# Optimization experiments

Hardware: AMD Instinct MI355X
Metric: run time of the kernel (lower is better)

Reference implementation:

```python
import jax, jax.numpy as jnp
import numpy as np

B, TED, G, N, E, MD, NOISE = 10000, 512, 64, 2000, 64000, 15, 128
PAC = 10
PACDIM = (TED + NOISE) * PAC  # 6400
D0, D1 = 1024, 512


def _linear_params(k, fan_in, fan_out):
    kw, kb = jax.random.split(k)
    lim = 1.0 / np.sqrt(fan_in)
    w = jax.random.uniform(kw, (fan_in, fan_out), minval=-lim, maxval=lim, dtype=jnp.float32)
    b = jax.random.uniform(kb, (fan_out,), minval=-lim, maxval=lim, dtype=jnp.float32)
    return w, b


def setup_inputs() -> dict:
    key = jax.random.key(0)
    ks = jax.random.split(key, 12)
    inp = {
        'input_': jax.random.normal(ks[0], (B, TED), dtype=jnp.float32),
        'graphs_x': jax.random.normal(ks[1], (G, N, 1), dtype=jnp.float32),
        'edge_index': jax.random.randint(ks[2], (G, 2, E), 0, N, dtype=jnp.int32),
        'graph_ids': jax.random.randint(ks[3], (B,), 0, G, dtype=jnp.int32),
        'chain': jax.random.normal(ks[4], (B, 1), dtype=jnp.float32),
        'metadata': jax.random.normal(ks[5], (B, MD), dtype=jnp.float32),
    }
    inp['gcn_w'], inp['gcn_b'] = _linear_params(ks[6], 1, 1)
    inp['meta_w'], inp['meta_b'] = _linear_params(ks[7], 1 + MD, 32)
    inp['gme_w'], inp['gme_b'] = _linear_params(ks[8], N + 32, NOISE)
    inp['seq_w0'], inp['seq_b0'] = _linear_params(ks[9], PACDIM, D0)
    inp['seq_w1'], inp['seq_b1'] = _linear_params(ks[10], D0, D1)
    inp['seq_w2'], inp['seq_b2'] = _linear_params(ks[11], D1, 1)
    return inp


def _gcn_one(x, ei, gcn_w, gcn_b):
    # GCNConv(1,1) with self-loops and symmetric normalization.
    loops = jnp.arange(N, dtype=ei.dtype)
    src = jnp.concatenate([ei[0], loops])
    dst = jnp.concatenate([ei[1], loops])
    deg = jax.ops.segment_sum(jnp.ones_like(src, dtype=x.dtype), dst, num_segments=N)
    dinv = jax.lax.rsqrt(deg)  # deg >= 1 due to self-loops
    norm = dinv[src] * dinv[dst]  # [E+N]
    xw = x @ gcn_w  # [N,1]
    msg = xw[src] * norm[:, None]
    out = jax.ops.segment_sum(msg, dst, num_segments=N) + gcn_b
    return out.reshape(-1)  # flatten -> [N]


def reference(input_, graphs_x, edge_index, graph_ids, chain, metadata,
              gcn_w, gcn_b, meta_w, meta_b, gme_w, gme_b,
              seq_w0, seq_b0, seq_w1, seq_b1, seq_w2, seq_b2):
    # per-unique-graph GCN, vectorized over G graphs
    gcn_out = jax.vmap(lambda x, ei: _gcn_one(x, ei, gcn_w, gcn_b))(graphs_x, edge_index)  # [G,N]
    graph_emb = gcn_out[graph_ids]  # gather: [B,N]
    all_meta = jnp.concatenate([chain, metadata], axis=1)  # [B,1+MD]
    meta_emb = jax.nn.relu(all_meta @ meta_w + meta_b)  # [B,32]
    noise = jnp.concatenate([graph_emb, meta_emb], axis=1) @ gme_w + gme_b  # [B,NOISE]
    h = jnp.concatenate([input_, noise], axis=1).reshape(-1, PACDIM)  # [B/PAC, PACDIM]
    h = jax.nn.leaky_relu(h @ seq_w0 + seq_b0, 0.2)  # dropout omitted (eval mode)
    h = jax.nn.leaky_relu(h @ seq_w1 + seq_b1, 0.2)
    return h @ seq_w2 + seq_b2  # [B/PAC, 1]
```

## Files before the change

kernel.cpp:

```cpp
#include <hip/hip_runtime.h>

typedef __bf16 bf16_t;
typedef __bf16 bf16x4 __attribute__((ext_vector_type(4)));
typedef __bf16 bf16x8 __attribute__((ext_vector_type(8)));
typedef float floatx4 __attribute__((ext_vector_type(4)));

#define G_GRAPHS 64
#define N_NODES 2000
#define N_EDGES 64000
#define BATCH 10000
#define TED_ 512
#define NOISE_ 128
#define PACDIM_ 6400
#define D0_ 1024
#define D1_ 512
#define MROWS 1000
#define ESPLIT 8
#define EPB (N_EDGES / ESPLIT)
#define S0 10
#define S1 8

#define PACK_BLKS 5000
#define META_BLKS 2500
#define TW0_BLKS  6400
#define TW1_BLKS  512

__device__ __forceinline__ void glds16(const void* g, void* l) {
    __builtin_amdgcn_global_load_lds(
        (__attribute__((address_space(1))) void*)(g),
        (__attribute__((address_space(3))) void*)(l), 16, 0, 0);
}

__global__ __launch_bounds__(256) void zero_kernel(float4* __restrict__ p, int n4) {
    int i = blockIdx.x * 256 + threadIdx.x;
    if (i < n4) p[i] = make_float4(0.f, 0.f, 0.f, 0.f);
}

__global__ __launch_bounds__(512) void deg_kernel(
    const int* __restrict__ edge_index, float* __restrict__ degs)
{
    __shared__ float h[N_NODES];
    const int g = blockIdx.y, s = blockIdx.x, tid = threadIdx.x;
    for (int n = tid; n < N_NODES; n += 512) h[n] = 0.f;
    __syncthreads();
    const int* dst = edge_index + (size_t)g * 2 * N_EDGES + N_EDGES + s * EPB;
    for (int e = tid; e < EPB; e += 512) atomicAdd(&h[dst[e]], 1.0f);
    __syncthreads();
    float* dg = degs + (size_t)g * N_NODES;
    for (int n = tid; n < N_NODES; n += 512) {
        float v = h[n];
        if (v != 0.f) atomicAdd(&dg[n], v);
    }
}

__global__ __launch_bounds__(512) void msg_kernel(
    const float* __restrict__ graphs_x, const int* __restrict__ edge_index,
    const float* __restrict__ degs, float* __restrict__ outs)
{
    __shared__ float xsl[N_NODES];
    __shared__ float dvl[N_NODES];
    __shared__ float oh[N_NODES];
    const int g = blockIdx.y, s = blockIdx.x, tid = threadIdx.x;
    const float* xg = graphs_x + (size_t)g * N_NODES;
    const float* dgg = degs + (size_t)g * N_NODES;
    for (int n = tid; n < N_NODES; n += 512) {
        xsl[n] = xg[n];
        dvl[n] = rsqrtf(dgg[n] + 1.0f);
        oh[n] = 0.f;
    }
    __syncthreads();
    const int* src = edge_index + (size_t)g * 2 * N_EDGES + s * EPB;
    const int* dst = src + N_EDGES;
    for (int e = tid; e < EPB; e += 512) {
        int ss = src[e], dd = dst[e];
        atomicAdd(&oh[dd], xsl[ss] * dvl[ss] * dvl[dd]);
    }
    __syncthreads();
    float* og = outs + (size_t)g * N_NODES;
    for (int n = tid; n < N_NODES; n += 512) {
        float v = oh[n];
        if (v != 0.f) atomicAdd(&og[n], v);
    }
}

__global__ __launch_bounds__(512) void gnoise_part_kernel(
    const float* __restrict__ graphs_x, const float* __restrict__ degs,
    const float* __restrict__ outs,
    const float* __restrict__ gcn_w, const float* __restrict__ gcn_b,
    const float* __restrict__ gme_w, float* __restrict__ gnoise)
{
    __shared__ float of[500];
    __shared__ float part[4][128];
    const int s = blockIdx.x, g = blockIdx.y, tid = threadIdx.x;
    const int nBase = s * 500;
    const float w = gcn_w[0], b = gcn_b[0];
    for (int n = tid; n < 500; n += 512) {
        int gn = nBase + n;
        float di2 = 1.0f / (degs[(size_t)g * N_NODES + gn] + 1.0f);
        of[n] = w * (outs[(size_t)g * N_NODES + gn]
                     + graphs_x[(size_t)g * N_NODES + gn] * di2) + b;
    }
    __syncthreads();
    const int j = tid & 127, ch = tid >> 7;
    float acc = 0.f;
    const int n0 = ch * 125;
    for (int n = n0; n < n0 + 125; n++)
        acc += of[n] * gme_w[(size_t)(nBase + n) * 128 + j];
    part[ch][j] = acc;
    __syncthreads();
    if (tid < 128)
        atomicAdd(&gnoise[(size_t)g * 128 + tid],
                  part[0][tid] + part[1][tid] + part[2][tid] + part[3][tid]);
}

__global__ __launch_bounds__(256) void prep_kernel(
    const float* __restrict__ in,
    const float* __restrict__ chain, const float* __restrict__ metadata,
    const int* __restrict__ graph_ids,
    const float* __restrict__ meta_w, const float* __restrict__ meta_b,
    const float* __restrict__ gme_w, const float* __restrict__ gme_b,
    const float* __restrict__ gnoise, bf16_t* __restrict__ A,
    const float* __restrict__ seq_w0, bf16_t* __restrict__ W0t,
    const float* __restrict__ seq_w1, bf16_t* __restrict__ W1t)
{
    __shared__ float t[32][33];
    const int blk = blockIdx.x;
    if (blk < PACK_BLKS) {
        int idx = blk * 256 + threadIdx.x;
        float4 v = ((const float4*)in)[idx];
        int b = idx >> 7;
        int c = (idx & 127) << 2;
        int r = b / 10, slot = b - r * 10;
        bf16x4 o = { (bf16_t)v.x, (bf16_t)v.y, (bf16_t)v.z, (bf16_t)v.w };
        *(bf16x4*)(A + (size_t)r * PACDIM_ + slot * 640 + c) = o;
        return;
    }
    if (blk < PACK_BLKS + META_BLKS) {
        int wid = ((blk - PACK_BLKS) * 256 + threadIdx.x) >> 6;
        int lane = threadIdx.x & 63;
        const int b = wid;
        float me = 0.f;
        if (lane < 32) {
            me = meta_b[lane] + chain[b] * meta_w[lane];
            for (int i = 1; i < 16; i++)
                me += metadata[(size_t)b * 15 + (i - 1)] * meta_w[(size_t)i * 32 + lane];
            me = me > 0.f ? me : 0.f;
        }
        const int gid = graph_ids[b];
        const int j1 = lane, j2 = lane + 64;
        float n1 = gnoise[(size_t)gid * 128 + j1] + gme_b[j1];
        float n2 = gnoise[(size_t)gid * 128 + j2] + gme_b[j2];
        for (int k = 0; k < 32; k++) {
            float mk = __shfl(me, k, 64);
            const float* wrow = gme_w + (size_t)(N_NODES + k) * 128;
            n1 += mk * wrow[j1];
            n2 += mk * wrow[j2];
        }
        int r = b / 10, slot = b - r * 10;
        bf16_t* dp = A + (size_t)r * PACDIM_ + slot * 640 + TED_;
        dp[j1] = (bf16_t)n1;
        dp[j2] = (bf16_t)n2;
        return;
    }
    const float* W; bf16_t* Wt; int R, C, c0, r0;
    if (blk < PACK_BLKS + META_BLKS + TW0_BLKS) {
        int local = blk - PACK_BLKS - META_BLKS;
        W = seq_w0; Wt = W0t; R = PACDIM_; C = D0_;
        c0 = (local & 31) * 32; r0 = (local >> 5) * 32;
    } else {
        int local = blk - PACK_BLKS - META_BLKS - TW0_BLKS;
        W = seq_w1; Wt = W1t; R = D0_; C = D1_;
        c0 = (local & 15) * 32; r0 = (local >> 4) * 32;
    }
    int tx = threadIdx.x & 31, ty = threadIdx.x >> 5;
    for (int yy = ty; yy < 32; yy += 8)
        t[yy][tx] = W[(size_t)(r0 + yy) * C + c0 + tx];
    __syncthreads();
    for (int yy = ty; yy < 32; yy += 8)
        Wt[(size_t)(c0 + yy) * R + r0 + tx] = (bf16_t)t[tx][yy];
}

__global__ __launch_bounds__(256) void gemm_bt_splitk_kernel(
    const bf16_t* __restrict__ A,
    const bf16_t* __restrict__ Bt,
    float* __restrict__ P,
    int M, int N, int K, int KS)
{
    __shared__ __align__(16) bf16_t As[128 * 32];
    __shared__ __align__(16) bf16_t Bs[128 * 32];
    const int tid = threadIdx.x;
    const int wave = tid >> 6;
    const int lane = tid & 63;
    const int mBase = blockIdx.y * 128;
    const int nBase = blockIdx.x * 128;
    const int z = blockIdx.z;
    const int Mp = gridDim.y * 128;
    const int wm = (wave & 1) * 64;
    const int wn = (wave >> 1) * 64;

    floatx4 acc[4][4] = {};

    const int c0 = tid, c1 = tid + 256;
    const int rA0 = c0 >> 2, k80 = (c0 & 3) * 8;
    const int rA1 = c1 >> 2, k81 = (c1 & 3) * 8;
    int gm0 = mBase + rA0; if (gm0 > M - 1) gm0 = M - 1;
    int gm1 = mBase + rA1; if (gm1 > M - 1) gm1 = M - 1;
    const bf16_t* aP0 = A + (size_t)gm0 * K + k80;
    const bf16_t* aP1 = A + (size_t)gm1 * K + k81;
    const bf16_t* bP0 = Bt + (size_t)(nBase + rA0) * K + k80;
    const bf16_t* bP1 = Bt + (size_t)(nBase + rA1) * K + k81;
    char* lA0 = (char*)As + wave * 1024;
    char* lA1 = (char*)As + 4096 + wave * 1024;
    char* lB0 = (char*)Bs + wave * 1024;
    char* lB1 = (char*)Bs + 4096 + wave * 1024;

    const int kq = (lane >> 4) * 8;
    const int mr = lane & 15;
    const bf16x8* ra[4]; const bf16x8* rb[4];
    for (int i = 0; i < 4; i++)
        ra[i] = (const bf16x8*)&As[(wm + i * 16 + mr) * 32 + kq];
    for (int j = 0; j < 4; j++)
        rb[j] = (const bf16x8*)&Bs[(wn + j * 16 + mr) * 32 + kq];

    const int kEnd = z * KS + KS;
    for (int k0 = z * KS; k0 < kEnd; k0 += 32) {
        __syncthreads();
        glds16(aP0 + k0, lA0);
        glds16(aP1 + k0, lA1);
        glds16(bP0 + k0, lB0);
        glds16(bP1 + k0, lB1);
        __syncthreads();
        bf16x8 af[4], bfr[4];
        for (int i = 0; i < 4; i++) af[i] = *ra[i];
        for (int j = 0; j < 4; j++) bfr[j] = *rb[j];
        for (int i = 0; i < 4; i++)
            for (int j = 0; j < 4; j++)
                acc[i][j] = __builtin_amdgcn_mfma_f32_16x16x32_bf16(
                    af[i], bfr[j], acc[i][j], 0, 0, 0);
    }

    float* Pz = P + (size_t)z * Mp * N;
    const int rq = (lane >> 4) * 4;
    const int cn = lane & 15;
    for (int j = 0; j < 4; j++) {
        int col = nBase + wn + j * 16 + cn;
        for (int i = 0; i < 4; i++)
            for (int r = 0; r < 4; r++) {
                int rowm = mBase + wm + i * 16 + rq + r;
                Pz[(size_t)rowm * N + col] = acc[i][j][r];
            }
    }
}

__global__ __launch_bounds__(256) void reduce_bias_leaky_kernel(
    const float* __restrict__ P, const float* __restrict__ bias,
    bf16_t* __restrict__ C, int M, int N, int Mp, int S)
{
    int idx = blockIdx.x * 256 + threadIdx.x;
    int total = M * (N >> 2);
    if (idx >= total) return;
    int nv = N >> 2;
    int r = idx / nv, c4 = (idx - r * nv) << 2;
    size_t off = (size_t)r * N + c4;
    size_t stride = (size_t)Mp * N;
    float4 v = *(const float4*)(P + off);
    for (int s = 1; s < S; s++) {
        float4 u = *(const float4*)(P + s * stride + off);
        v.x += u.x; v.y += u.y; v.z += u.z; v.w += u.w;
    }
    const float4 bv = *(const float4*)(bias + c4);
    v.x += bv.x; v.y += bv.y; v.z += bv.z; v.w += bv.w;
    v.x = v.x > 0.f ? v.x : 0.2f * v.x;
    v.y = v.y > 0.f ? v.y : 0.2f * v.y;
    v.z = v.z > 0.f ? v.z : 0.2f * v.z;
    v.w = v.w > 0.f ? v.w : 0.2f * v.w;
    bf16x4 o = { (bf16_t)v.x, (bf16_t)v.y, (bf16_t)v.z, (bf16_t)v.w };
    *(bf16x4*)(C + off) = o;
}

__global__ __launch_bounds__(256) void final_fused_kernel(
    const float* __restrict__ P, const float* __restrict__ b1,
    const float* __restrict__ w2, const float* __restrict__ b2,
    float* __restrict__ out, int Mp, int S)
{
    int wid = (blockIdx.x * 256 + threadIdx.x) >> 6;
    int lane = threadIdx.x & 63;
    if (wid >= MROWS) return;
    size_t stride = (size_t)Mp * D1_;
    const float* base = P + (size_t)wid * D1_;
    float s = 0.f;
    for (int i = 0; i < 8; i++) {
        int c = i * 64 + lane;
        float v = base[c];
        for (int z = 1; z < S; z++) v += base[(size_t)z * stride + c];
        v += b1[c];
        v = v > 0.f ? v : 0.2f * v;
        s += v * w2[c];
    }
    for (int off = 32; off; off >>= 1) s += __shfl_down(s, off, 64);
    if (lane == 0) out[wid] = s + b2[0];
}

extern "C" void kernel_launch(void* const* d_in, const int* in_sizes, int n_in,
                              void* d_out, int out_size, void* d_ws, size_t ws_size,
                              hipStream_t stream)
{
    const float* input_    = (const float*)d_in[0];
    const float* graphs_x  = (const float*)d_in[1];
    const int*   edge_idx  = (const int*)  d_in[2];
    const int*   graph_ids = (const int*)  d_in[3];
    const float* chain     = (const float*)d_in[4];
    const float* metadata  = (const float*)d_in[5];
    const float* gcn_w     = (const float*)d_in[6];
    const float* gcn_b     = (const float*)d_in[7];
    const float* meta_w    = (const float*)d_in[8];
    const float* meta_b    = (const float*)d_in[9];
    const float* gme_w     = (const float*)d_in[10];
    const float* gme_b     = (const float*)d_in[11];
    const float* seq_w0    = (const float*)d_in[12];
    const float* seq_b0    = (const float*)d_in[13];
    const float* seq_w1    = (const float*)d_in[14];
    const float* seq_b1    = (const float*)d_in[15];
    const float* seq_w2    = (const float*)d_in[16];
    const float* seq_b2    = (const float*)d_in[17];
    float* out = (float*)d_out;

    char* ws = (char*)d_ws;
    float*  gnoise = (float*)(ws + 0);
    float*  degs   = (float*)(ws + 32768);
    float*  outs   = (float*)(ws + 544768);
    bf16_t* Abuf   = (bf16_t*)(ws + 1056768);
    bf16_t* W0t    = (bf16_t*)(ws + 13856768);
    bf16_t* W1t    = (bf16_t*)(ws + 26963968);
    bf16_t* H1     = (bf16_t*)(ws + 28012544);
    float*  P      = (float*)(ws + 30060544);

    const int zn4 = (32768 + 512000 + 512000) / 16;
    zero_kernel<<<(zn4 + 255) / 256, 256, 0, stream>>>((float4*)gnoise, zn4);
    deg_kernel<<<dim3(ESPLIT, G_GRAPHS), 512, 0, stream>>>(edge_idx, degs);
    msg_kernel<<<dim3(ESPLIT, G_GRAPHS), 512, 0, stream>>>(graphs_x, edge_idx, degs, outs);
    gnoise_part_kernel<<<dim3(4, G_GRAPHS), 512, 0, stream>>>(
        graphs_x, degs, outs, gcn_w, gcn_b, gme_w, gnoise);

    prep_kernel<<<PACK_BLKS + META_BLKS + TW0_BLKS + TW1_BLKS, 256, 0, stream>>>(
        input_, chain, metadata, graph_ids, meta_w, meta_b, gme_w, gme_b,
        gnoise, Abuf, seq_w0, W0t, seq_w1, W1t);

    gemm_bt_splitk_kernel<<<dim3(D0_ / 128, 8, S0), 256, 0, stream>>>(
        Abuf, W0t, P, MROWS, D0_, PACDIM_, PACDIM_ / S0);
    reduce_bias_leaky_kernel<<<(MROWS * D0_ / 4 + 255) / 256, 256, 0, stream>>>(
        P, seq_b0, H1, MROWS, D0_, 1024, S0);

    gemm_bt_splitk_kernel<<<dim3(D1_ / 128, 8, S1), 256, 0, stream>>>(
        H1, W1t, P, MROWS, D1_, D0_, D0_ / S1);
    final_fused_kernel<<<(MROWS * 64 + 255) / 256, 256, 0, stream>>>(
        P, seq_b1, seq_w2, seq_b2, out, 1024, S1);
}
```

Measured before the change: 277.6 us.

## Fuse GCN front-end and prep stages into one cooperative persistent kernel

Replaces the zero, degree, message, graph-noise and prep kernels with a single cooperative kernel of 256 blocks that uses grid-wide syncs between phases. The weight transposes and input packing are done in grid-stride loops before the first sync. The intent is to remove several kernel launches and the gaps between them. The risk is lower parallelism in each phase, especially the large weight transpose, plus the cost of the grid barriers.

```diff
diff --git a/kernel.cpp b/kernel.cpp
--- a/kernel.cpp
+++ b/kernel.cpp
@@ -1,4 +1,7 @@
 #include <hip/hip_runtime.h>
+#include <hip/hip_cooperative_groups.h>
+
+namespace cg = cooperative_groups;
 
 typedef __bf16 bf16_t;
 typedef __bf16 bf16x4 __attribute__((ext_vector_type(4)));
@@ -15,15 +18,13 @@
 #define D0_ 1024
 #define D1_ 512
 #define MROWS 1000
-#define ESPLIT 8
-#define EPB (N_EDGES / ESPLIT)
 #define S0 10
 #define S1 8
 
-#define PACK_BLKS 5000
-#define META_BLKS 2500
-#define TW0_BLKS  6400
-#define TW1_BLKS  512
+#define FBLOCKS 256
+#define EPB4 (N_EDGES / 4)
+#define TW0_TILES 6400
+#define TW1_TILES 512
 
 __device__ __forceinline__ void glds16(const void* g, void* l) {
     __builtin_amdgcn_global_load_lds(
@@ -31,160 +32,155 @@
         (__attribute__((address_space(3))) void*)(l), 16, 0, 0);
 }
 
-__global__ __launch_bounds__(256) void zero_kernel(float4* __restrict__ p, int n4) {
-    int i = blockIdx.x * 256 + threadIdx.x;
-    if (i < n4) p[i] = make_float4(0.f, 0.f, 0.f, 0.f);
-}
-
-__global__ __launch_bounds__(512) void deg_kernel(
-    const int* __restrict__ edge_index, float* __restrict__ degs)
-{
-    __shared__ float h[N_NODES];
-    const int g = blockIdx.y, s = blockIdx.x, tid = threadIdx.x;
-    for (int n = tid; n < N_NODES; n += 512) h[n] = 0.f;
-    __syncthreads();
-    const int* dst = edge_index + (size_t)g * 2 * N_EDGES + N_EDGES + s * EPB;
-    for (int e = tid; e < EPB; e += 512) atomicAdd(&h[dst[e]], 1.0f);
-    __syncthreads();
-    float* dg = degs + (size_t)g * N_NODES;
-    for (int n = tid; n < N_NODES; n += 512) {
-        float v = h[n];
-        if (v != 0.f) atomicAdd(&dg[n], v);
-    }
-}
-
-__global__ __launch_bounds__(512) void msg_kernel(
+__global__ __launch_bounds__(512) void fused_front_kernel(
+    const float* __restrict__ input_,
     const float* __restrict__ graphs_x, const int* __restrict__ edge_index,
-    const float* __restrict__ degs, float* __restrict__ outs)
-{
-    __shared__ float xsl[N_NODES];
-    __shared__ float dvl[N_NODES];
-    __shared__ float oh[N_NODES];
-    const int g = blockIdx.y, s = blockIdx.x, tid = threadIdx.x;
-    const float* xg = graphs_x + (size_t)g * N_NODES;
-    const float* dgg = degs + (size_t)g * N_NODES;
-    for (int n = tid; n < N_NODES; n += 512) {
-        xsl[n] = xg[n];
-        dvl[n] = rsqrtf(dgg[n] + 1.0f);
-        oh[n] = 0.f;
-    }
-    __syncthreads();
-    const int* src = edge_index + (size_t)g * 2 * N_EDGES + s * EPB;
-    const int* dst = src + N_EDGES;
-    for (int e = tid; e < EPB; e += 512) {
-        int ss = src[e], dd = dst[e];
-        atomicAdd(&oh[dd], xsl[ss] * dvl[ss] * dvl[dd]);
-    }
-    __syncthreads();
-    float* og = outs + (size_t)g * N_NODES;
-    for (int n = tid; n < N_NODES; n += 512) {
-        float v = oh[n];
-        if (v != 0.f) atomicAdd(&og[n], v);
-    }
-}
-
-__global__ __launch_bounds__(512) void gnoise_part_kernel(
-    const float* __restrict__ graphs_x, const float* __restrict__ degs,
-    const float* __restrict__ outs,
+    const int* __restrict__ graph_ids, const float* __restrict__ chain,
+    const float* __restrict__ metadata,
     const float* __restrict__ gcn_w, const float* __restrict__ gcn_b,
-    const float* __restrict__ gme_w, float* __restrict__ gnoise)
-{
-    __shared__ float of[500];
-    __shared__ float part[4][128];
-    const int s = blockIdx.x, g = blockIdx.y, tid = threadIdx.x;
-    const int nBase = s * 500;
-    const float w = gcn_w[0], b = gcn_b[0];
-    for (int n = tid; n < 500; n += 512) {
-        int gn = nBase + n;
-        float di2 = 1.0f / (degs[(size_t)g * N_NODES + gn] + 1.0f);
-        of[n] = w * (outs[(size_t)g * N_NODES + gn]
-                     + graphs_x[(size_t)g * N_NODES + gn] * di2) + b;
-    }
-    __syncthreads();
-    const int j = tid & 127, ch = tid >> 7;
-    float acc = 0.f;
-    const int n0 = ch * 125;
-    for (int n = n0; n < n0 + 125; n++)
-        acc += of[n] * gme_w[(size_t)(nBase + n) * 128 + j];
-    part[ch][j] = acc;
-    __syncthreads();
-    if (tid < 128)
-        atomicAdd(&gnoise[(size_t)g * 128 + tid],
-                  part[0][tid] + part[1][tid] + part[2][tid] + part[3][tid]);
-}
-
-__global__ __launch_bounds__(256) void prep_kernel(
-    const float* __restrict__ in,
-    const float* __restrict__ chain, const float* __restrict__ metadata,
-    const int* __restrict__ graph_ids,
     const float* __restrict__ meta_w, const float* __restrict__ meta_b,
     const float* __restrict__ gme_w, const float* __restrict__ gme_b,
-    const float* __restrict__ gnoise, bf16_t* __restrict__ A,
-    const float* __restrict__ seq_w0, bf16_t* __restrict__ W0t,
-    const float* __restrict__ seq_w1, bf16_t* __restrict__ W1t)
-{
-    __shared__ float t[32][33];
-    const int blk = blockIdx.x;
-    if (blk < PACK_BLKS) {
-        int idx = blk * 256 + threadIdx.x;
-        float4 v = ((const float4*)in)[idx];
+    const float* __restrict__ seq_w0, const float* __restrict__ seq_w1,
+    float* __restrict__ degs, float* __restrict__ outs, float* __restrict__ gnoise,
+    bf16_t* __restrict__ A, bf16_t* __restrict__ W0t, bf16_t* __restrict__ W1t)
+{
+    cg::grid_group grid = cg::this_grid();
+    __shared__ float smem[6000];
+    const int tid = threadIdx.x, blk = blockIdx.x;
+    const int gtid = blk * 512 + tid;
+
+    {
+        float4* z = (float4*)gnoise;
+        if (gtid < 66048) z[gtid] = make_float4(0.f, 0.f, 0.f, 0.f);
+    }
+    for (int idx = gtid; idx < BATCH * TED_ / 4; idx += FBLOCKS * 512) {
+        float4 v = ((const float4*)input_)[idx];
         int b = idx >> 7;
         int c = (idx & 127) << 2;
         int r = b / 10, slot = b - r * 10;
         bf16x4 o = { (bf16_t)v.x, (bf16_t)v.y, (bf16_t)v.z, (bf16_t)v.w };
         *(bf16x4*)(A + (size_t)r * PACDIM_ + slot * 640 + c) = o;
-        return;
-    }
-    if (blk < PACK_BLKS + META_BLKS) {
-        int wid = ((blk - PACK_BLKS) * 256 + threadIdx.x) >> 6;
-        int lane = threadIdx.x & 63;
-        const int b = wid;
-        float me = 0.f;
-        if (lane < 32) {
-            me = meta_b[lane] + chain[b] * meta_w[lane];
-            for (int i = 1; i < 16; i++)
-                me += metadata[(size_t)b * 15 + (i - 1)] * meta_w[(size_t)i * 32 + lane];
-            me = me > 0.f ? me : 0.f;
-        }
-        const int gid = graph_ids[b];
-        const int j1 = lane, j2 = lane + 64;
-        float n1 = gnoise[(size_t)gid * 128 + j1] + gme_b[j1];
-        float n2 = gnoise[(size_t)gid * 128 + j2] + gme_b[j2];
-        for (int k = 0; k < 32; k++) {
-            float mk = __shfl(me, k, 64);
-            const float* wrow = gme_w + (size_t)(N_NODES + k) * 128;
-            n1 += mk * wrow[j1];
-            n2 += mk * wrow[j2];
-        }
-        int r = b / 10, slot = b - r * 10;
-        bf16_t* dp = A + (size_t)r * PACDIM_ + slot * 640 + TED_;
-        dp[j1] = (bf16_t)n1;
-        dp[j2] = (bf16_t)n2;
-        return;
-    }
-    const float* W; bf16_t* Wt; int R, C, c0, r0;
-    if (blk < PACK_BLKS + META_BLKS + TW0_BLKS) {
-        int local = blk - PACK_BLKS - META_BLKS;
-        W = seq_w0; Wt = W0t; R = PACDIM_; C = D0_;
-        c0 = (local & 31) * 32; r0 = (local >> 5) * 32;
-    } else {
-        int local = blk - PACK_BLKS - META_BLKS - TW0_BLKS;
-        W = seq_w1; Wt = W1t; R = D0_; C = D1_;
-        c0 = (local & 15) * 32; r0 = (local >> 4) * 32;
-    }
-    int tx = threadIdx.x & 31, ty = threadIdx.x >> 5;
-    for (int yy = ty; yy < 32; yy += 8)
-        t[yy][tx] = W[(size_t)(r0 + yy) * C + c0 + tx];
-    __syncthreads();
-    for (int yy = ty; yy < 32; yy += 8)
-        Wt[(size_t)(c0 + yy) * R + r0 + tx] = (bf16_t)t[tx][yy];
+    }
+    {
+        int tx = tid & 31, ty = tid >> 5;
+        float (*t)[33] = (float(*)[33])smem;
+        for (int tile = blk; tile < TW0_TILES + TW1_TILES; tile += FBLOCKS) {
+            const float* W; bf16_t* Wt; int R, C, c0, r0;
+            if (tile < TW0_TILES) {
+                W = seq_w0; Wt = W0t; R = PACDIM_; C = D0_;
+                c0 = (tile & 31) * 32; r0 = (tile >> 5) * 32;
+            } else {
+                int l = tile - TW0_TILES;
+                W = seq_w1; Wt = W1t; R = D0_; C = D1_;
+                c0 = (l & 15) * 32; r0 = (l >> 4) * 32;
+            }
+            __syncthreads();
+            for (int yy = ty; yy < 32; yy += 16)
+                t[yy][tx] = W[(size_t)(r0 + yy) * C + c0 + tx];
+            __syncthreads();
+            for (int yy = ty; yy < 32; yy += 16)
+                Wt[(size_t)(c0 + yy) * R + r0 + tx] = (bf16_t)t[tx][yy];
+        }
+    }
+    grid.sync();
+    {
+        const int g = blk >> 2, s = blk & 3;
+        float* h = smem;
+        for (int n = tid; n < N_NODES; n += 512) h[n] = 0.f;
+        __syncthreads();
+        const int* dst = edge_index + (size_t)g * 2 * N_EDGES + N_EDGES + s * EPB4;
+        for (int e = tid; e < EPB4; e += 512) atomicAdd(&h[dst[e]], 1.0f);
+        __syncthreads();
+        float* dg = degs + (size_t)g * N_NODES;
+        for (int n = tid; n < N_NODES; n += 512) {
+            float v = h[n];
+            if (v != 0.f) atomicAdd(&dg[n], v);
+        }
+    }
+    grid.sync();
+    {
+        const int g = blk >> 2, s = blk & 3;
+        float* xsl = smem;
+        float* dvl = smem + 2000;
+        float* oh  = smem + 4000;
+        const float* xg = graphs_x + (size_t)g * N_NODES;
+        const float* dgg = degs + (size_t)g * N_NODES;
+        for (int n = tid; n < N_NODES; n += 512) {
+            xsl[n] = xg[n];
+            dvl[n] = rsqrtf(dgg[n] + 1.0f);
+            oh[n] = 0.f;
+        }
+        __syncthreads();
+        const int* src = edge_index + (size_t)g * 2 * N_EDGES + s * EPB4;
+        const int* dst = src + N_EDGES;
+        for (int e = tid; e < EPB4; e += 512) {
+            int ss = src[e], dd = dst[e];
+            atomicAdd(&oh[dd], xsl[ss] * dvl[ss] * dvl[dd]);
+        }
+        __syncthreads();
+        float* og = outs + (size_t)g * N_NODES;
+        for (int n = tid; n < N_NODES; n += 512) {
+            float v = oh[n];
+            if (v != 0.f) atomicAdd(&og[n], v);
+        }
+    }
+    grid.sync();
+    {
+        const int g = blk >> 2, s = blk & 3;
+        const int nBase = s * 500;
+        float* of = smem;
+        float* part = smem + 512;
+        const float w = gcn_w[0], b = gcn_b[0];
+        for (int n = tid; n < 500; n += 512) {
+            int gn = nBase + n;
+            float di2 = 1.0f / (degs[(size_t)g * N_NODES + gn] + 1.0f);
+            of[n] = w * (outs[(size_t)g * N_NODES + gn]
+                         + graphs_x[(size_t)g * N_NODES + gn] * di2) + b;
+        }
+        __syncthreads();
+        const int j = tid & 127, ch = tid >> 7;
+        float acc = 0.f;
+        for (int n = ch; n < 500; n += 4)
+            acc += of[n] * gme_w[(size_t)(nBase + n) * 128 + j];
+        part[ch * 128 + j] = acc;
+        __syncthreads();
+        if (tid < 128)
+            atomicAdd(&gnoise[(size_t)g * 128 + tid],
+                      part[tid] + part[128 + tid] + part[256 + tid] + part[384 + tid]);
+    }
+    grid.sync();
+    {
+        const int lane = tid & 63;
+        for (int wid = blk * 8 + (tid >> 6); wid < BATCH; wid += FBLOCKS * 8) {
+            const int b = wid;
+            float me = 0.f;
+            if (lane < 32) {
+                me = meta_b[lane] + chain[b] * meta_w[lane];
+                for (int i = 1; i < 16; i++)
+                    me += metadata[(size_t)b * 15 + (i - 1)] * meta_w[(size_t)i * 32 + lane];
+                me = me > 0.f ? me : 0.f;
+            }
+            const int gid = graph_ids[b];
+            const int j1 = lane, j2 = lane + 64;
+            float n1 = gnoise[(size_t)gid * 128 + j1] + gme_b[j1];
+            float n2 = gnoise[(size_t)gid * 128 + j2] + gme_b[j2];
+            for (int k = 0; k < 32; k++) {
+                float mk = __shfl(me, k, 64);
+                const float* wrow = gme_w + (size_t)(N_NODES + k) * 128;
+                n1 += mk * wrow[j1];
+                n2 += mk * wrow[j2];
+            }
+            int r = b / 10, slot = b - r * 10;
+            bf16_t* dp = A + (size_t)r * PACDIM_ + slot * 640 + TED_;
+            dp[j1] = (bf16_t)n1;
+            dp[j2] = (bf16_t)n2;
+        }
+    }
 }
 
 __global__ __launch_bounds__(256) void gemm_bt_splitk_kernel(
-    const bf16_t* __restrict__ A,
-    const bf16_t* __restrict__ Bt,
-    float* __restrict__ P,
-    int M, int N, int K, int KS)
+    const bf16_t* __restrict__ A, const bf16_t* __restrict__ Bt,
+    float* __restrict__ P, int M, int N, int K, int KS)
 {
     __shared__ __align__(16) bf16_t As[128 * 32];
     __shared__ __align__(16) bf16_t Bs[128 * 32];
@@ -335,16 +331,16 @@
     bf16_t* H1     = (bf16_t*)(ws + 28012544);
     float*  P      = (float*)(ws + 30060544);
 
-    const int zn4 = (32768 + 512000 + 512000) / 16;
-    zero_kernel<<<(zn4 + 255) / 256, 256, 0, stream>>>((float4*)gnoise, zn4);
-    deg_kernel<<<dim3(ESPLIT, G_GRAPHS), 512, 0, stream>>>(edge_idx, degs);
-    msg_kernel<<<dim3(ESPLIT, G_GRAPHS), 512, 0, stream>>>(graphs_x, edge_idx, degs, outs);
-    gnoise_part_kernel<<<dim3(4, G_GRAPHS), 512, 0, stream>>>(
-        graphs_x, degs, outs, gcn_w, gcn_b, gme_w, gnoise);
-
-    prep_kernel<<<PACK_BLKS + META_BLKS + TW0_BLKS + TW1_BLKS, 256, 0, stream>>>(
-        input_, chain, metadata, graph_ids, meta_w, meta_b, gme_w, gme_b,
-        gnoise, Abuf, seq_w0, W0t, seq_w1, W1t);
+    void* kargs[] = {
+        (void*)&input_, (void*)&graphs_x, (void*)&edge_idx, (void*)&graph_ids,
+        (void*)&chain, (void*)&metadata, (void*)&gcn_w, (void*)&gcn_b,
+        (void*)&meta_w, (void*)&meta_b, (void*)&gme_w, (void*)&gme_b,
+        (void*)&seq_w0, (void*)&seq_w1,
+        (void*)&degs, (void*)&outs, (void*)&gnoise,
+        (void*)&Abuf, (void*)&W0t, (void*)&W1t
+    };
+    hipLaunchCooperativeKernel((const void*)fused_front_kernel,
+                               dim3(FBLOCKS), dim3(512), kargs, 0, stream);
 
     gemm_bt_splitk_kernel<<<dim3(D0_ / 128, 8, S0), 256, 0, stream>>>(
         Abuf, W0t, P, MROWS, D0_, PACDIM_, PACDIM_ / S0);
```

After: 472.0 us. +70.0%, slower.
